# Kernel tuning notes

Hardware: AMD Instinct MI355X
Metric: run time of the kernel (lower is better)

## Reference

```python
import jax, jax.numpy as jnp
import numpy as np

# Model dims (match init_kwargs)
INPUT_CAPS = 2048
INPUT_DIM = 16
OUTPUT_CAPS = 16
OUTPUT_DIM = 16
D = OUTPUT_CAPS * OUTPUT_DIM  # 256
BATCH = 64


def setup_inputs() -> dict:
    key = jax.random.key(0)
    k1, k2 = jax.random.split(key)
    caps_output = jax.random.normal(k1, (BATCH, INPUT_CAPS, INPUT_DIM), dtype=jnp.float32)
    stdv = 1.0 / np.sqrt(INPUT_CAPS)
    weights = jax.random.uniform(k2, (INPUT_CAPS, INPUT_DIM, D),
                                 minval=-stdv, maxval=stdv, dtype=jnp.float32)
    return {"caps_output": caps_output, "weights": weights}


def reference(caps_output, weights):
    # u_predict[b,c,:] = caps_output[b,c,:] @ weights[c]  -> [B, IC, D]
    u = jnp.einsum('bci,cio->bco', caps_output, weights)
    # Gram matrix C = A^T A  -> [B, D, D], symmetric PSD (real eigenvalues)
    C = jnp.einsum('bcd,bce->bde', u, u)
    # Top eigenpair. Original code uses np.linalg.eig per batch on CPU and
    # selects the largest eigenvalue; C is symmetric so eigh is the faithful
    # (and efficient) form. eigh returns ascending order -> take last column.
    e_vals, e_vecs = jnp.linalg.eigh(C)
    v = e_vecs[:, :, -1]  # [B, D] dominant eigenvector
    # Fix eigenvector sign deterministically (largest-|component| positive)
    idx = jnp.argmax(jnp.abs(v), axis=1)
    sgn = jnp.sign(jnp.take_along_axis(v, idx[:, None], axis=1))
    v = v * sgn
    return v.reshape(BATCH, OUTPUT_CAPS, OUTPUT_DIM)
```

## Files before the change

### kernel.cpp

```cpp
#include <hip/hip_runtime.h>

#define NB  64
#define IC  2048
#define ID  16
#define DD  256
#define DDSQ 65536
#define PB  (DDSQ * NB)
#define NSQ 11
#define NPI 7

typedef __attribute__((ext_vector_type(8))) short          s16x8;
typedef __attribute__((ext_vector_type(4))) float          f32x4;
typedef __attribute__((ext_vector_type(4))) unsigned short us4;
typedef __attribute__((ext_vector_type(8))) unsigned short us8;

__device__ __forceinline__ unsigned short f2b(float f) {
    union { float f; unsigned u; } c; c.f = f;
    const unsigned u = c.u + 0x7FFFu + ((c.u >> 16) & 1u);
    return (unsigned short)(u >> 16);
}
__device__ __forceinline__ float b2f(unsigned short h) {
    union { unsigned u; float f; } c; c.u = ((unsigned)h) << 16;
    return c.f;
}
__device__ __forceinline__ unsigned f2pk(float f) {
    const unsigned short h = f2b(f);
    const unsigned short l = f2b(f - b2f(h));
    return ((unsigned)h << 16) | (unsigned)l;
}

__global__ __launch_bounds__(256, 4) void u_kernel(const float* __restrict__ caps,
                                                   const float* __restrict__ W,
                                                   unsigned* __restrict__ U) {
    const int c = blockIdx.x;
    const int t = threadIdx.x;
    __shared__ float xsT[ID][64];
    {
        const int b = t >> 2, q = (t & 3) * 4;
        const float4 x4 = *(const float4*)&caps[((size_t)b * IC + c) * ID + q];
        xsT[q + 0][b] = x4.x; xsT[q + 1][b] = x4.y;
        xsT[q + 2][b] = x4.z; xsT[q + 3][b] = x4.w;
    }
    __syncthreads();
    float a[64];
#pragma unroll
    for (int b = 0; b < 64; ++b) a[b] = 0.f;
#pragma unroll
    for (int i = 0; i < ID; ++i) {
        const float wi = W[((size_t)c * ID + i) * DD + t];
#pragma unroll
        for (int g = 0; g < 16; ++g) {
            const float4 x = *(const float4*)&xsT[i][g * 4];
            a[g * 4 + 0] = fmaf(x.x, wi, a[g * 4 + 0]);
            a[g * 4 + 1] = fmaf(x.y, wi, a[g * 4 + 1]);
            a[g * 4 + 2] = fmaf(x.z, wi, a[g * 4 + 2]);
            a[g * 4 + 3] = fmaf(x.w, wi, a[g * 4 + 3]);
        }
    }
#pragma unroll
    for (int b = 0; b < 64; ++b)
        U[((size_t)b * IC + c) * DD + t] = f2pk(a[b]);
}

__global__ __launch_bounds__(256, 2)
void cmb_kernel(const unsigned* __restrict__ Up,
                unsigned short* __restrict__ Ch, unsigned short* __restrict__ Cl,
                float* __restrict__ Sc) {
    const int id   = blockIdx.x;
    const int bb   = id & 63;
    const int tile = id >> 6;
    const int tr = tile >> 2, tc = tile & 3;
    const int d0 = tr * 128, e0 = tc * 64;
    const int t    = threadIdx.x;
    const int lane = t & 63, wid = t >> 6;
    const int wm = wid >> 1, wn = wid & 1;
    const int fr = lane & 15, kg = lane >> 4;
    const int sl8 = lane & 7, qg = lane >> 3;
    const size_t mb = (size_t)bb * DDSQ;

    __shared__ unsigned short Ah[128][40];
    __shared__ unsigned short Al[128][40];
    __shared__ unsigned short Bh[64][40];
    __shared__ unsigned short Bl[64][40];
    __shared__ float red[256];

    const f32x4 z4 = {0.f, 0.f, 0.f, 0.f};
    f32x4 acc[4][2];
#pragma unroll
    for (int m = 0; m < 4; ++m)
#pragma unroll
        for (int n = 0; n < 2; ++n) acc[m][n] = z4;

    const unsigned* Ub = Up + (size_t)bb * IC * DD;
    unsigned va[4][4], vb[2][4];
    auto loadU = [&](int kb) {
#pragma unroll
        for (int s = 0; s < 4; ++s) {
            const int row = wid * 8 + sl8 + 32 * s;
#pragma unroll
            for (int j = 0; j < 4; ++j)
                va[s][j] = Ub[(size_t)(kb + 4 * qg + j) * DD + d0 + row];
        }
#pragma unroll
        for (int s = 0; s < 2; ++s) {
            const int row = wid * 8 + sl8 + 32 * s;
#pragma unroll
            for (int j = 0; j < 4; ++j)
                vb[s][j] = Ub[(size_t)(kb + 4 * qg + j) * DD + e0 + row];
        }
    };

    loadU(0);
    for (int kb = 0; kb < IC; kb += 32) {
        __syncthreads();
#pragma unroll
        for (int s = 0; s < 4; ++s) {
            const int row = wid * 8 + sl8 + 32 * s;
            us4 h, l;
#pragma unroll
            for (int j = 0; j < 4; ++j) {
                h[j] = (unsigned short)(va[s][j] >> 16);
                l[j] = (unsigned short)(va[s][j] & 0xFFFFu);
            }
            *(us4*)&Ah[row][4 * qg] = h;
            *(us4*)&Al[row][4 * qg] = l;
        }
#pragma unroll
        for (int s = 0; s < 2; ++s) {
            const int row = wid * 8 + sl8 + 32 * s;
            us4 h, l;
#pragma unroll
            for (int j = 0; j < 4; ++j) {
                h[j] = (unsigned short)(vb[s][j] >> 16);
                l[j] = (unsigned short)(vb[s][j] & 0xFFFFu);
            }
            *(us4*)&Bh[row][4 * qg] = h;
            *(us4*)&Bl[row][4 * qg] = l;
        }
        __syncthreads();
        if (kb + 32 < IC) loadU(kb + 32);
        s16x8 ah[4], al[4], bh[2], bl[2];
#pragma unroll
        for (int m = 0; m < 4; ++m) {
            const int r = wm * 64 + m * 16 + fr;
            ah[m] = *(const s16x8*)&Ah[r][kg * 8];
            al[m] = *(const s16x8*)&Al[r][kg * 8];
        }
#pragma unroll
        for (int n = 0; n < 2; ++n) {
            const int r = wn * 32 + n * 16 + fr;
            bh[n] = *(const s16x8*)&Bh[r][kg * 8];
            bl[n] = *(const s16x8*)&Bl[r][kg * 8];
        }
#pragma unroll
        for (int m = 0; m < 4; ++m)
#pragma unroll
            for (int n = 0; n < 2; ++n) {
                acc[m][n] = __builtin_amdgcn_mfma_f32_16x16x32_bf16(ah[m], bh[n], acc[m][n], 0, 0, 0);
                acc[m][n] = __builtin_amdgcn_mfma_f32_16x16x32_bf16(ah[m], bl[n], acc[m][n], 0, 0, 0);
                acc[m][n] = __builtin_amdgcn_mfma_f32_16x16x32_bf16(al[m], bh[n], acc[m][n], 0, 0, 0);
            }
    }

    float ts = 0.f;
    const int row_l = wm * 64 + (lane >> 4) * 4;
    const int col_l = wn * 32 + fr;
#pragma unroll
    for (int m = 0; m < 4; ++m)
#pragma unroll
        for (int n = 0; n < 2; ++n)
#pragma unroll
            for (int r = 0; r < 4; ++r) {
                const int gr = d0 + row_l + m * 16 + r;
                const int gc = e0 + col_l + n * 16;
                const float e = acc[m][n][r];
                const unsigned short h = f2b(e);
                const unsigned short l = f2b(e - b2f(h));
                const size_t o = mb + (size_t)gr * DD + gc;
                Ch[o] = h; Cl[o] = l;
                if (gr == gc) ts += e;
            }
    if ((tc >> 1) == tr) {
        red[t] = ts;
        __syncthreads();
        for (int s2 = 128; s2 > 0; s2 >>= 1) {
            if (t < s2) red[t] += red[t + s2];
            __syncthreads();
        }
        if (t == 0) atomicAdd(&Sc[bb], red[0]);
    }
}

__global__ __launch_bounds__(256, 4)
void sqm_kernel(const unsigned short* __restrict__ Dh, const unsigned short* __restrict__ Dl,
                unsigned short* __restrict__ Eh, unsigned short* __restrict__ El,
                const float* __restrict__ s_in, float* __restrict__ s_out) {
    const int id   = blockIdx.x;
    const int bb   = id & 63;
    const int tile = id >> 6;
    int tr, tc;
    if (tile < 4)      { tr = 0; tc = tile; }
    else if (tile < 7) { tr = 1; tc = tile - 3; }
    else if (tile < 9) { tr = 2; tc = tile - 5; }
    else               { tr = 3; tc = 3; }
    const int d0 = tr * 64, e0 = tc * 64;
    const int t    = threadIdx.x;
    const int lane = t & 63, wid = t >> 6;
    const int wm = wid >> 1, wn = wid & 1;
    const int fr = lane & 15, kg = lane >> 4;
    const size_t mb = (size_t)bb * DDSQ;

    __shared__ unsigned short Ah[64][72];
    __shared__ unsigned short Al[64][72];
    __shared__ unsigned short Bh[64][72];
    __shared__ unsigned short Bl[64][72];
    __shared__ float red[256];

    const f32x4 z4 = {0.f, 0.f, 0.f, 0.f};
    f32x4 acc[2][2];
#pragma unroll
    for (int m = 0; m < 2; ++m)
#pragma unroll
        for (int n = 0; n < 2; ++n) acc[m][n] = z4;

    const float s   = s_in[bb];
    const float inv = 1.f / (s * s);
    const int row = t >> 2, q = t & 3;

    for (int kb = 0; kb < DD; kb += 64) {
        const size_t ga = mb + (size_t)(d0 + row) * DD + kb + q * 8;
        const size_t gb = mb + (size_t)(e0 + row) * DD + kb + q * 8;
        const int4 rah0 = *(const int4*)&Dh[ga];
        const int4 rah1 = *(const int4*)&Dh[ga + 32];
        const int4 ral0 = *(const int4*)&Dl[ga];
        const int4 ral1 = *(const int4*)&Dl[ga + 32];
        const int4 rbh0 = *(const int4*)&Dh[gb];
        const int4 rbh1 = *(const int4*)&Dh[gb + 32];
        const int4 rbl0 = *(const int4*)&Dl[gb];
        const int4 rbl1 = *(const int4*)&Dl[gb + 32];
        __syncthreads();
        *(int4*)&Ah[row][q * 8]      = rah0;
        *(int4*)&Ah[row][q * 8 + 32] = rah1;
        *(int4*)&Al[row][q * 8]      = ral0;
        *(int4*)&Al[row][q * 8 + 32] = ral1;
        *(int4*)&Bh[row][q * 8]      = rbh0;
        *(int4*)&Bh[row][q * 8 + 32] = rbh1;
        *(int4*)&Bl[row][q * 8]      = rbl0;
        *(int4*)&Bl[row][q * 8 + 32] = rbl1;
        __syncthreads();

#pragma unroll
        for (int h = 0; h < 2; ++h) {
            const int ko = kg * 8 + 32 * h;
            s16x8 ah[2], al[2], bh[2], bl[2];
#pragma unroll
            for (int m = 0; m < 2; ++m) {
                const int r = wm * 32 + m * 16 + fr;
                ah[m] = *(const s16x8*)&Ah[r][ko];
                al[m] = *(const s16x8*)&Al[r][ko];
            }
#pragma unroll
            for (int n = 0; n < 2; ++n) {
                const int r = wn * 32 + n * 16 + fr;
                bh[n] = *(const s16x8*)&Bh[r][ko];
                bl[n] = *(const s16x8*)&Bl[r][ko];
            }
#pragma unroll
            for (int m = 0; m < 2; ++m)
#pragma unroll
                for (int n = 0; n < 2; ++n) {
                    acc[m][n] = __builtin_amdgcn_mfma_f32_16x16x32_bf16(ah[m], bh[n], acc[m][n], 0, 0, 0);
                    acc[m][n] = __builtin_amdgcn_mfma_f32_16x16x32_bf16(ah[m], bl[n], acc[m][n], 0, 0, 0);
                    acc[m][n] = __builtin_amdgcn_mfma_f32_16x16x32_bf16(al[m], bh[n], acc[m][n], 0, 0, 0);
                }
        }
    }

    float ts = 0.f;
    const int row_l = wm * 32 + (lane >> 4) * 4;
    const int col_l = wn * 32 + fr;
    const bool mir = (tr != tc);
#pragma unroll
    for (int m = 0; m < 2; ++m)
#pragma unroll
        for (int n = 0; n < 2; ++n) {
            const int gr0 = d0 + row_l + m * 16;
            const int gc  = e0 + col_l + n * 16;
            us4 h4, l4;
#pragma unroll
            for (int r = 0; r < 4; ++r) {
                const float e = acc[m][n][r] * inv;
                const unsigned short h = f2b(e);
                const unsigned short l = f2b(e - b2f(h));
                const size_t o = mb + (size_t)(gr0 + r) * DD + gc;
                Eh[o] = h; El[o] = l;
                h4[r] = h; l4[r] = l;
                if (gr0 + r == gc) ts += e;
            }
            if (mir) {
                const size_t o2 = mb + (size_t)gc * DD + gr0;
                *(us4*)&Eh[o2] = h4;
                *(us4*)&El[o2] = l4;
            }
        }
    if (tr == tc) {
        red[t] = ts;
        __syncthreads();
        for (int s2 = 128; s2 > 0; s2 >>= 1) {
            if (t < s2) red[t] += red[t + s2];
            __syncthreads();
        }
        if (t == 0) atomicAdd(&s_out[bb], red[0]);
    }
}

__global__ __launch_bounds__(256, 2) void finish_kernel(const unsigned short* __restrict__ Dh,
                                                        const unsigned short* __restrict__ Dl,
                                                        float* __restrict__ out) {
    const int b = blockIdx.x, t = threadIdx.x;
    const size_t mb = (size_t)b * DDSQ;
    __shared__ float vs[DD];
    __shared__ float red[DD];
    __shared__ int   ridx[DD];
    red[t] = b2f(Dh[mb + (size_t)t * DD + t]) + b2f(Dl[mb + (size_t)t * DD + t]);
    ridx[t] = t;
    __syncthreads();
    for (int s = 128; s > 0; s >>= 1) {
        if (t < s && red[t + s] > red[t]) { red[t] = red[t + s]; ridx[t] = ridx[t + s]; }
        __syncthreads();
    }
    const int jmax0 = ridx[0];
    __syncthreads();
    float v = b2f(Dh[mb + (size_t)jmax0 * DD + t]) + b2f(Dl[mb + (size_t)jmax0 * DD + t]);
    for (int it = 0; it < NPI; ++it) {
        vs[t] = v;
        __syncthreads();
        float a = 0.f;
        const unsigned short* rh = Dh + mb + (size_t)t * DD;
        const unsigned short* rl = Dl + mb + (size_t)t * DD;
#pragma unroll 4
        for (int j = 0; j < DD; j += 8) {
            const us8 h8 = *(const us8*)&rh[j];
            const us8 l8 = *(const us8*)&rl[j];
            a = fmaf(b2f(h8[0]) + b2f(l8[0]), vs[j + 0], a);
            a = fmaf(b2f(h8[1]) + b2f(l8[1]), vs[j + 1], a);
            a = fmaf(b2f(h8[2]) + b2f(l8[2]), vs[j + 2], a);
            a = fmaf(b2f(h8[3]) + b2f(l8[3]), vs[j + 3], a);
            a = fmaf(b2f(h8[4]) + b2f(l8[4]), vs[j + 4], a);
            a = fmaf(b2f(h8[5]) + b2f(l8[5]), vs[j + 5], a);
            a = fmaf(b2f(h8[6]) + b2f(l8[6]), vs[j + 6], a);
            a = fmaf(b2f(h8[7]) + b2f(l8[7]), vs[j + 7], a);
        }
        __syncthreads();
        v = a;
    }
    vs[t] = v;
    red[t] = v * v;
    __syncthreads();
    for (int s = 128; s > 0; s >>= 1) {
        if (t < s) red[t] += red[t + s];
        __syncthreads();
    }
    const float nrm = sqrtf(red[0]);
    __syncthreads();
    red[t] = fabsf(v);
    ridx[t] = t;
    __syncthreads();
    for (int s = 128; s > 0; s >>= 1) {
        if (t < s && red[t + s] > red[t]) { red[t] = red[t + s]; ridx[t] = ridx[t + s]; }
        __syncthreads();
    }
    const float sgn = (vs[ridx[0]] < 0.f) ? -1.f : 1.f;
    out[(size_t)b * DD + t] = sgn * v / nrm;
}

extern "C" void kernel_launch(void* const* d_in, const int* in_sizes, int n_in,
                              void* d_out, int out_size, void* d_ws, size_t ws_size,
                              hipStream_t stream) {
    const float* caps = (const float*)d_in[0];
    const float* W    = (const float*)d_in[1];
    float* out = (float*)d_out;
    float* ws  = (float*)d_ws;

    unsigned* Up = (unsigned*)ws;
    unsigned short* Xh = (unsigned short*)(ws + (size_t)8 * PB);
    unsigned short* Xl = Xh + (size_t)NB * DDSQ;
    unsigned short* Yh = (unsigned short*)(ws + (size_t)9 * PB);
    unsigned short* Yl = Yh + (size_t)NB * DDSQ;
    float* Sc = ws + (size_t)10 * PB;

    hipMemsetAsync(Sc, 0, 2048 * sizeof(float), stream);

    u_kernel<<<IC, 256, 0, stream>>>(caps, W, Up);
    cmb_kernel<<<512, 256, 0, stream>>>(Up, Xh, Xl, Sc);

    unsigned short* ph = Xh; unsigned short* pl = Xl;
    unsigned short* qh = Yh; unsigned short* ql = Yl;
    for (int it = 0; it < NSQ; ++it) {
        sqm_kernel<<<640, 256, 0, stream>>>(ph, pl, qh, ql,
                                            Sc + it * 64, Sc + (it + 1) * 64);
        unsigned short* t1 = ph; ph = qh; qh = t1;
        unsigned short* t2 = pl; pl = ql; ql = t2;
    }

    finish_kernel<<<NB, 256, 0, stream>>>(ph, pl, out);
}
```

Measured before the change: 371.4 us.

## Fuse repeated squaring launches and finish into one persistent kernel with grid barrier

Replaces the eleven separate matrix-squaring launches and the final power-iteration kernel with a single persistent kernel of 512 blocks. The blocks synchronise through an atomic-counter grid barrier between squaring steps. Each block now computes two full 64x64 tiles per step instead of using the upper-triangle tiling with mirrored stores, so it no longer exploits symmetry. The aim is to remove launch gaps and tail effects, at the cost of doing all 16 tiles, relying on every block being co-resident, and spinning on the barrier.

```diff
diff --git a/kernel.cpp b/kernel.cpp
--- a/kernel.cpp
+++ b/kernel.cpp
@@ -191,23 +191,30 @@
     }
 }
 
-__global__ __launch_bounds__(256, 4)
-void sqm_kernel(const unsigned short* __restrict__ Dh, const unsigned short* __restrict__ Dl,
-                unsigned short* __restrict__ Eh, unsigned short* __restrict__ El,
-                const float* __restrict__ s_in, float* __restrict__ s_out) {
-    const int id   = blockIdx.x;
-    const int bb   = id & 63;
-    const int tile = id >> 6;
-    int tr, tc;
-    if (tile < 4)      { tr = 0; tc = tile; }
-    else if (tile < 7) { tr = 1; tc = tile - 3; }
-    else if (tile < 9) { tr = 2; tc = tile - 5; }
-    else               { tr = 3; tc = 3; }
-    const int d0 = tr * 64, e0 = tc * 64;
+__device__ __forceinline__ void grid_sync(unsigned* bar, unsigned target) {
+    __syncthreads();
+    if (threadIdx.x == 0) {
+        __threadfence();
+        atomicAdd(bar, 1u);
+        while (atomicAdd(bar, 0u) < target)
+            __builtin_amdgcn_s_sleep(64);
+    }
+    __syncthreads();
+    __threadfence();
+}
+
+__global__ __launch_bounds__(256, 2)
+void sqc_kernel(unsigned short* __restrict__ Xh, unsigned short* __restrict__ Xl,
+                unsigned short* __restrict__ Yh, unsigned short* __restrict__ Yl,
+                float* __restrict__ Sc, unsigned* __restrict__ bar,
+                float* __restrict__ out) {
+    const int blk  = blockIdx.x;
     const int t    = threadIdx.x;
     const int lane = t & 63, wid = t >> 6;
     const int wm = wid >> 1, wn = wid & 1;
     const int fr = lane & 15, kg = lane >> 4;
+    const int row = t >> 2, q = t & 3;
+    const int bb = blk & 63;
     const size_t mb = (size_t)bb * DDSQ;
 
     __shared__ unsigned short Ah[64][72];
@@ -217,161 +224,165 @@
     __shared__ float red[256];
 
     const f32x4 z4 = {0.f, 0.f, 0.f, 0.f};
-    f32x4 acc[2][2];
-#pragma unroll
-    for (int m = 0; m < 2; ++m)
-#pragma unroll
-        for (int n = 0; n < 2; ++n) acc[m][n] = z4;
-
-    const float s   = s_in[bb];
-    const float inv = 1.f / (s * s);
-    const int row = t >> 2, q = t & 3;
-
-    for (int kb = 0; kb < DD; kb += 64) {
-        const size_t ga = mb + (size_t)(d0 + row) * DD + kb + q * 8;
-        const size_t gb = mb + (size_t)(e0 + row) * DD + kb + q * 8;
-        const int4 rah0 = *(const int4*)&Dh[ga];
-        const int4 rah1 = *(const int4*)&Dh[ga + 32];
-        const int4 ral0 = *(const int4*)&Dl[ga];
-        const int4 ral1 = *(const int4*)&Dl[ga + 32];
-        const int4 rbh0 = *(const int4*)&Dh[gb];
-        const int4 rbh1 = *(const int4*)&Dh[gb + 32];
-        const int4 rbl0 = *(const int4*)&Dl[gb];
-        const int4 rbl1 = *(const int4*)&Dl[gb + 32];
-        __syncthreads();
-        *(int4*)&Ah[row][q * 8]      = rah0;
-        *(int4*)&Ah[row][q * 8 + 32] = rah1;
-        *(int4*)&Al[row][q * 8]      = ral0;
-        *(int4*)&Al[row][q * 8 + 32] = ral1;
-        *(int4*)&Bh[row][q * 8]      = rbh0;
-        *(int4*)&Bh[row][q * 8 + 32] = rbh1;
-        *(int4*)&Bl[row][q * 8]      = rbl0;
-        *(int4*)&Bl[row][q * 8 + 32] = rbl1;
-        __syncthreads();
-
-#pragma unroll
-        for (int h = 0; h < 2; ++h) {
-            const int ko = kg * 8 + 32 * h;
-            s16x8 ah[2], al[2], bh[2], bl[2];
-#pragma unroll
-            for (int m = 0; m < 2; ++m) {
-                const int r = wm * 32 + m * 16 + fr;
-                ah[m] = *(const s16x8*)&Ah[r][ko];
-                al[m] = *(const s16x8*)&Al[r][ko];
-            }
-#pragma unroll
-            for (int n = 0; n < 2; ++n) {
-                const int r = wn * 32 + n * 16 + fr;
-                bh[n] = *(const s16x8*)&Bh[r][ko];
-                bl[n] = *(const s16x8*)&Bl[r][ko];
-            }
+
+    for (int it = 0; it < NSQ; ++it) {
+        const unsigned short* dh = (it & 1) ? Yh : Xh;
+        const unsigned short* dl = (it & 1) ? Yl : Xl;
+        unsigned short* eh = (it & 1) ? Xh : Yh;
+        unsigned short* el = (it & 1) ? Xl : Yl;
+        const float s   = Sc[it * 64 + bb];
+        const float inv = 1.f / (s * s);
+        float* s_out = Sc + (it + 1) * 64;
+
+#pragma unroll 1
+        for (int j = 0; j < 2; ++j) {
+            const int tile = (blk >> 6) + j * 8;
+            const int tr = tile >> 2, tc = tile & 3;
+            const int d0 = tr * 64, e0 = tc * 64;
+
+            f32x4 acc[2][2];
 #pragma unroll
             for (int m = 0; m < 2; ++m)
 #pragma unroll
-                for (int n = 0; n < 2; ++n) {
-                    acc[m][n] = __builtin_amdgcn_mfma_f32_16x16x32_bf16(ah[m], bh[n], acc[m][n], 0, 0, 0);
-                    acc[m][n] = __builtin_amdgcn_mfma_f32_16x16x32_bf16(ah[m], bl[n], acc[m][n], 0, 0, 0);
-                    acc[m][n] = __builtin_amdgcn_mfma_f32_16x16x32_bf16(al[m], bh[n], acc[m][n], 0, 0, 0);
+                for (int n = 0; n < 2; ++n) acc[m][n] = z4;
+
+            for (int kb = 0; kb < DD; kb += 64) {
+                const size_t ga = mb + (size_t)(d0 + row) * DD + kb + q * 8;
+                const size_t gb = mb + (size_t)(e0 + row) * DD + kb + q * 8;
+                const int4 rah0 = *(const int4*)&dh[ga];
+                const int4 rah1 = *(const int4*)&dh[ga + 32];
+                const int4 ral0 = *(const int4*)&dl[ga];
+                const int4 ral1 = *(const int4*)&dl[ga + 32];
+                const int4 rbh0 = *(const int4*)&dh[gb];
+                const int4 rbh1 = *(const int4*)&dh[gb + 32];
+                const int4 rbl0 = *(const int4*)&dl[gb];
+                const int4 rbl1 = *(const int4*)&dl[gb + 32];
+                __syncthreads();
+                *(int4*)&Ah[row][q * 8]      = rah0;
+                *(int4*)&Ah[row][q * 8 + 32] = rah1;
+                *(int4*)&Al[row][q * 8]      = ral0;
+                *(int4*)&Al[row][q * 8 + 32] = ral1;
+                *(int4*)&Bh[row][q * 8]      = rbh0;
+                *(int4*)&Bh[row][q * 8 + 32] = rbh1;
+                *(int4*)&Bl[row][q * 8]      = rbl0;
+                *(int4*)&Bl[row][q * 8 + 32] = rbl1;
+                __syncthreads();
+
+#pragma unroll
+                for (int h = 0; h < 2; ++h) {
+                    const int ko = kg * 8 + 32 * h;
+                    s16x8 ah[2], al[2], bh[2], bl[2];
+#pragma unroll
+                    for (int m = 0; m < 2; ++m) {
+                        const int r = wm * 32 + m * 16 + fr;
+                        ah[m] = *(const s16x8*)&Ah[r][ko];
+                        al[m] = *(const s16x8*)&Al[r][ko];
+                    }
+#pragma unroll
+                    for (int n = 0; n < 2; ++n) {
+                        const int r = wn * 32 + n * 16 + fr;
+                        bh[n] = *(const s16x8*)&Bh[r][ko];
+                        bl[n] = *(const s16x8*)&Bl[r][ko];
+                    }
+#pragma unroll
+                    for (int m = 0; m < 2; ++m)
+#pragma unroll
+                        for (int n = 0; n < 2; ++n) {
+                            acc[m][n] = __builtin_amdgcn_mfma_f32_16x16x32_bf16(ah[m], bh[n], acc[m][n], 0, 0, 0);
+                            acc[m][n] = __builtin_amdgcn_mfma_f32_16x16x32_bf16(ah[m], bl[n], acc[m][n], 0, 0, 0);
+                            acc[m][n] = __builtin_amdgcn_mfma_f32_16x16x32_bf16(al[m], bh[n], acc[m][n], 0, 0, 0);
+                        }
                 }
-        }
-    }
-
-    float ts = 0.f;
-    const int row_l = wm * 32 + (lane >> 4) * 4;
-    const int col_l = wn * 32 + fr;
-    const bool mir = (tr != tc);
-#pragma unroll
-    for (int m = 0; m < 2; ++m)
-#pragma unroll
-        for (int n = 0; n < 2; ++n) {
-            const int gr0 = d0 + row_l + m * 16;
-            const int gc  = e0 + col_l + n * 16;
-            us4 h4, l4;
-#pragma unroll
-            for (int r = 0; r < 4; ++r) {
-                const float e = acc[m][n][r] * inv;
-                const unsigned short h = f2b(e);
-                const unsigned short l = f2b(e - b2f(h));
-                const size_t o = mb + (size_t)(gr0 + r) * DD + gc;
-                Eh[o] = h; El[o] = l;
-                h4[r] = h; l4[r] = l;
-                if (gr0 + r == gc) ts += e;
-            }
-            if (mir) {
-                const size_t o2 = mb + (size_t)gc * DD + gr0;
-                *(us4*)&Eh[o2] = h4;
-                *(us4*)&El[o2] = l4;
-            }
-        }
-    if (tr == tc) {
-        red[t] = ts;
+            }
+
+            float ts = 0.f;
+            const int row_l = wm * 32 + (lane >> 4) * 4;
+            const int col_l = wn * 32 + fr;
+#pragma unroll
+            for (int m = 0; m < 2; ++m)
+#pragma unroll
+                for (int n = 0; n < 2; ++n)
+#pragma unroll
+                    for (int r = 0; r < 4; ++r) {
+                        const int gr = d0 + row_l + m * 16 + r;
+                        const int gc = e0 + col_l + n * 16;
+                        const float e = acc[m][n][r] * inv;
+                        const unsigned short h = f2b(e);
+                        const unsigned short l = f2b(e - b2f(h));
+                        const size_t o = mb + (size_t)gr * DD + gc;
+                        eh[o] = h; el[o] = l;
+                        if (gr == gc) ts += e;
+                    }
+            if (tr == tc) {
+                red[t] = ts;
+                __syncthreads();
+                for (int s2 = 128; s2 > 0; s2 >>= 1) {
+                    if (t < s2) red[t] += red[t + s2];
+                    __syncthreads();
+                }
+                if (t == 0) atomicAdd(&s_out[bb], red[0]);
+            }
+        }
+        grid_sync(bar, 512u * (unsigned)(it + 1));
+    }
+
+    if (blk < 64) {
+        const unsigned short* Fh = Yh;
+        const unsigned short* Fl = Yl;
+        const size_t fb = (size_t)blk * DDSQ;
+        float* vs  = (float*)&Ah[0][0];
+        int*  ridx = (int*)&Bh[0][0];
+        red[t] = b2f(Fh[fb + (size_t)t * DD + t]) + b2f(Fl[fb + (size_t)t * DD + t]);
+        ridx[t] = t;
+        __syncthreads();
+        for (int s2 = 128; s2 > 0; s2 >>= 1) {
+            if (t < s2 && red[t + s2] > red[t]) { red[t] = red[t + s2]; ridx[t] = ridx[t + s2]; }
+            __syncthreads();
+        }
+        const int jmax0 = ridx[0];
+        __syncthreads();
+        float v = b2f(Fh[fb + (size_t)jmax0 * DD + t]) + b2f(Fl[fb + (size_t)jmax0 * DD + t]);
+        for (int itv = 0; itv < NPI; ++itv) {
+            vs[t] = v;
+            __syncthreads();
+            float a = 0.f;
+            const unsigned short* rh = Fh + fb + (size_t)t * DD;
+            const unsigned short* rl = Fl + fb + (size_t)t * DD;
+#pragma unroll 4
+            for (int j = 0; j < DD; j += 8) {
+                const us8 h8 = *(const us8*)&rh[j];
+                const us8 l8 = *(const us8*)&rl[j];
+                a = fmaf(b2f(h8[0]) + b2f(l8[0]), vs[j + 0], a);
+                a = fmaf(b2f(h8[1]) + b2f(l8[1]), vs[j + 1], a);
+                a = fmaf(b2f(h8[2]) + b2f(l8[2]), vs[j + 2], a);
+                a = fmaf(b2f(h8[3]) + b2f(l8[3]), vs[j + 3], a);
+                a = fmaf(b2f(h8[4]) + b2f(l8[4]), vs[j + 4], a);
+                a = fmaf(b2f(h8[5]) + b2f(l8[5]), vs[j + 5], a);
+                a = fmaf(b2f(h8[6]) + b2f(l8[6]), vs[j + 6], a);
+                a = fmaf(b2f(h8[7]) + b2f(l8[7]), vs[j + 7], a);
+            }
+            __syncthreads();
+            v = a;
+        }
+        vs[t] = v;
+        red[t] = v * v;
         __syncthreads();
         for (int s2 = 128; s2 > 0; s2 >>= 1) {
             if (t < s2) red[t] += red[t + s2];
             __syncthreads();
         }
-        if (t == 0) atomicAdd(&s_out[bb], red[0]);
-    }
-}
-
-__global__ __launch_bounds__(256, 2) void finish_kernel(const unsigned short* __restrict__ Dh,
-                                                        const unsigned short* __restrict__ Dl,
-                                                        float* __restrict__ out) {
-    const int b = blockIdx.x, t = threadIdx.x;
-    const size_t mb = (size_t)b * DDSQ;
-    __shared__ float vs[DD];
-    __shared__ float red[DD];
-    __shared__ int   ridx[DD];
-    red[t] = b2f(Dh[mb + (size_t)t * DD + t]) + b2f(Dl[mb + (size_t)t * DD + t]);
-    ridx[t] = t;
-    __syncthreads();
-    for (int s = 128; s > 0; s >>= 1) {
-        if (t < s && red[t + s] > red[t]) { red[t] = red[t + s]; ridx[t] = ridx[t + s]; }
-        __syncthreads();
-    }
-    const int jmax0 = ridx[0];
-    __syncthreads();
-    float v = b2f(Dh[mb + (size_t)jmax0 * DD + t]) + b2f(Dl[mb + (size_t)jmax0 * DD + t]);
-    for (int it = 0; it < NPI; ++it) {
-        vs[t] = v;
-        __syncthreads();
-        float a = 0.f;
-        const unsigned short* rh = Dh + mb + (size_t)t * DD;
-        const unsigned short* rl = Dl + mb + (size_t)t * DD;
-#pragma unroll 4
-        for (int j = 0; j < DD; j += 8) {
-            const us8 h8 = *(const us8*)&rh[j];
-            const us8 l8 = *(const us8*)&rl[j];
-            a = fmaf(b2f(h8[0]) + b2f(l8[0]), vs[j + 0], a);
-            a = fmaf(b2f(h8[1]) + b2f(l8[1]), vs[j + 1], a);
-            a = fmaf(b2f(h8[2]) + b2f(l8[2]), vs[j + 2], a);
-            a = fmaf(b2f(h8[3]) + b2f(l8[3]), vs[j + 3], a);
-            a = fmaf(b2f(h8[4]) + b2f(l8[4]), vs[j + 4], a);
-            a = fmaf(b2f(h8[5]) + b2f(l8[5]), vs[j + 5], a);
-            a = fmaf(b2f(h8[6]) + b2f(l8[6]), vs[j + 6], a);
-            a = fmaf(b2f(h8[7]) + b2f(l8[7]), vs[j + 7], a);
-        }
-        __syncthreads();
-        v = a;
-    }
-    vs[t] = v;
-    red[t] = v * v;
-    __syncthreads();
-    for (int s = 128; s > 0; s >>= 1) {
-        if (t < s) red[t] += red[t + s];
-        __syncthreads();
-    }
-    const float nrm = sqrtf(red[0]);
-    __syncthreads();
-    red[t] = fabsf(v);
-    ridx[t] = t;
-    __syncthreads();
-    for (int s = 128; s > 0; s >>= 1) {
-        if (t < s && red[t + s] > red[t]) { red[t] = red[t + s]; ridx[t] = ridx[t + s]; }
-        __syncthreads();
-    }
-    const float sgn = (vs[ridx[0]] < 0.f) ? -1.f : 1.f;
-    out[(size_t)b * DD + t] = sgn * v / nrm;
+        const float nrm = sqrtf(red[0]);
+        __syncthreads();
+        red[t] = fabsf(v);
+        ridx[t] = t;
+        __syncthreads();
+        for (int s2 = 128; s2 > 0; s2 >>= 1) {
+            if (t < s2 && red[t + s2] > red[t]) { red[t] = red[t + s2]; ridx[t] = ridx[t + s2]; }
+            __syncthreads();
+        }
+        const float sgn = (vs[ridx[0]] < 0.f) ? -1.f : 1.f;
+        out[(size_t)blk * DD + t] = sgn * v / nrm;
+    }
 }
 
 extern "C" void kernel_launch(void* const* d_in, const int* in_sizes, int n_in,
@@ -388,20 +399,12 @@
     unsigned short* Yh = (unsigned short*)(ws + (size_t)9 * PB);
     unsigned short* Yl = Yh + (size_t)NB * DDSQ;
     float* Sc = ws + (size_t)10 * PB;
+    unsigned* bar = (unsigned*)(Sc + 1024);
 
     hipMemsetAsync(Sc, 0, 2048 * sizeof(float), stream);
 
     u_kernel<<<IC, 256, 0, stream>>>(caps, W, Up);
     cmb_kernel<<<512, 256, 0, stream>>>(Up, Xh, Xl, Sc);
 
-    unsigned short* ph = Xh; unsigned short* pl = Xl;
-    unsigned short* qh = Yh; unsigned short* ql = Yl;
-    for (int it = 0; it < NSQ; ++it) {
-        sqm_kernel<<<640, 256, 0, stream>>>(ph, pl, qh, ql,
-                                            Sc + it * 64, Sc + (it + 1) * 64);
-        unsigned short* t1 = ph; ph = qh; qh = t1;
-        unsigned short* t2 = pl; pl = ql; ql = t2;
-    }
-
-    finish_kernel<<<NB, 256, 0, stream>>>(ph, pl, out);
-}
+    sqc_kernel<<<512, 256, 0, stream>>>(Xh, Xl, Yh, Yl, Sc, bar, out);
+}
```

Measured after the change: 1.307 ms. 3.52x slower.
